# Kernel tuning notes

Hardware: AMD Instinct MI355X
Metric: run time of the kernel (lower is better)

Reference implementation:

```python
import jax, jax.numpy as jnp
import numpy as np

L, D, H, KV, HD, KVL, I, PL = 8, 2048, 8, 2, 256, 4096, 8192, 256
FULL = (4,)          # layers with full (global) attention / global RoPE
POS = 2047           # current decode position (cache write slot)
N_REP = H // KV      # GQA expansion factor


def rms(x, eps=1e-6):
    # RMSNorm without scale (v_norm); scale applied by caller where needed
    return x * jax.lax.rsqrt(jnp.mean(x * x, axis=-1, keepdims=True) + eps)


def rope(x, cos, sin):
    half = HD // 2
    rot = jnp.concatenate([-x[..., half:], x[..., :half]], axis=-1)
    return x * cos + rot * sin


def _rope_tables(theta):
    inv = 1.0 / (theta ** (np.arange(0, HD, 2, dtype=np.float32) / HD))
    ang = jnp.asarray(POS * inv, dtype=jnp.float32)
    return jnp.concatenate([jnp.cos(ang)] * 2), jnp.concatenate([jnp.sin(ang)] * 2)


def setup_inputs() -> dict:
    key = jax.random.key(0)
    ks = jax.random.split(key, 24)
    r = lambda k, s, sc=0.02: jax.random.normal(k, s, jnp.float32) * sc
    gains = lambda k, s: 1.0 + jax.random.normal(k, s, jnp.float32) * 0.02
    cos_s, sin_s = _rope_tables(10000.0)
    cos_f, sin_f = _rope_tables(1000000.0)
    um = jnp.zeros((1, 1, KVL, 1), jnp.float32).at[0, 0, POS, 0].set(1.0)
    mask = jnp.where(jnp.arange(KVL) <= POS, 0.0, -1e9).astype(jnp.float32)
    return {
        "hidden_states": r(ks[0], (1, 1, D), 1.0),
        "causal_mask": mask,
        "update_mask": um,
        "per_layer_combined": r(ks[1], (1, 1, L * PL), 1.0),
        "cos_s": cos_s, "sin_s": sin_s, "cos_f": cos_f, "sin_f": sin_f,
        "K_in": r(ks[2], (L, KV, KVL, HD)),
        "V_in": r(ks[3], (L, KV, KVL, HD)),
        "w_q": r(ks[4], (L, H * HD, D)),
        "w_k": r(ks[5], (L, KV * HD, D)),
        "w_v": r(ks[6], (L, KV * HD, D)),
        "w_o": r(ks[7], (L, D, H * HD)),
        "g_in_ln": gains(ks[8], (L, D)),
        "g_q_norm": gains(ks[9], (L, HD)),
        "g_k_norm": gains(ks[10], (L, HD)),
        "g_post_attn_ln": gains(ks[11], (L, D)),
        "g_pre_ff_ln": gains(ks[12], (L, D)),
        "g_post_ff_ln": gains(ks[13], (L, D)),
        "w_gate": r(ks[14], (L, I, D)),
        "w_up": r(ks[15], (L, I, D)),
        "w_down": r(ks[16], (L, D, I)),
        "w_plg": r(ks[17], (L, PL, D)),
        "w_plp": r(ks[18], (L, D, PL)),
        "g_post_pl_ln": gains(ks[19], (L, D)),
        "layer_scalar": jnp.ones((L,), jnp.float32),
    }


def reference(hidden_states, causal_mask, update_mask, per_layer_combined,
              cos_s, sin_s, cos_f, sin_f, K_in, V_in,
              w_q, w_k, w_v, w_o,
              g_in_ln, g_q_norm, g_k_norm, g_post_attn_ln, g_pre_ff_ln, g_post_ff_ln,
              w_gate, w_up, w_down, w_plg, w_plp, g_post_pl_ln, layer_scalar):
    um = update_mask[0, 0]          # [KVL,1] one-hot at write position
    h = hidden_states[0, 0]         # [D], batch=1/seq=1 decode
    K_outs, V_outs = [], []
    for i in range(L):
        cos, sin = (cos_f, sin_f) if i in FULL else (cos_s, sin_s)
        # --- attention block ---
        res = h
        x = rms(h) * g_in_ln[i]
        q = rms((w_q[i] @ x).reshape(H, HD)) * g_q_norm[i]
        q = rope(q, cos, sin)                                   # [H,HD]
        k = rms((w_k[i] @ x).reshape(KV, HD)) * g_k_norm[i]
        k = rope(k, cos, sin)                                   # [KV,HD]
        v = rms((w_v[i] @ x).reshape(KV, HD))                    # v_norm (no scale)
        # full-tensor masked blend = KV cache write (faithful to source)
        Ko = K_in[i] * (1.0 - um) + k[:, None, :] * um          # [KV,KVL,HD]
        Vo = V_in[i] * (1.0 - um) + v[:, None, :] * um
        K_outs.append(Ko); V_outs.append(Vo)
        Ke = jnp.repeat(Ko, N_REP, axis=0)                      # GQA expand [H,KVL,HD]
        Ve = jnp.repeat(Vo, N_REP, axis=0)
        scores = jnp.einsum('hd,hkd->hk', q, Ke) + causal_mask  # no 1/sqrt(hd) in source
        attn = jax.nn.softmax(scores, axis=-1)
        ao = jnp.einsum('hk,hkd->hd', attn, Ve).reshape(H * HD)
        ao = rms(w_o[i] @ ao) * g_post_attn_ln[i]
        h = res + ao
        # --- gated MLP ---
        res = h
        xm = rms(h) * g_pre_ff_ln[i]
        m = w_down[i] @ (jax.nn.gelu(w_gate[i] @ xm, approximate=True) * (w_up[i] @ xm))
        h = res + rms(m) * g_post_ff_ln[i]
        # --- per-layer input gating ---
        res = h
        pls = per_layer_combined[0, 0, i * PL:(i + 1) * PL]     # [PL]
        g = jax.nn.gelu(w_plg[i] @ h, approximate=True) * pls
        h = res + rms(w_plp[i] @ g) * g_post_pl_ln[i]
        h = h * layer_scalar[i]
    return (h[None, None, :], jnp.stack(K_outs), jnp.stack(V_outs))
```

## Files before the change

kernel.cpp:

```cpp
#include <hip/hip_runtime.h>

#define NL   8
#define DIM  2048
#define NH   8
#define NKV  2
#define HD   256
#define KVL  4096
#define FFI  8192
#define PLD  256
#define POS  2047
#define NCH  128
#define CP   16

__device__ __forceinline__ float dot4(float4 a, float4 b){
  return a.x*b.x + a.y*b.y + a.z*b.z + a.w*b.w;
}

__device__ __forceinline__ float waveAllSum(float v){
#pragma unroll
  for(int o=1;o<64;o<<=1) v += __shfl_xor(v,o,64);
  return v;
}

__device__ __forceinline__ float blockSum256(float v, float* red){
  int lane = threadIdx.x & 63, w = threadIdx.x >> 6;
  v = waveAllSum(v);
  __syncthreads();
  if(lane==0) red[w] = v;
  __syncthreads();
  return red[0]+red[1]+red[2]+red[3];
}

__device__ __forceinline__ float gelu_tanh(float v){
  return 0.5f*v*(1.0f + tanhf(0.7978845608028654f*(v + 0.044715f*v*v*v)));
}

__device__ __forceinline__ float4 normRope(const float* __restrict__ raw, int lane,
    const float* __restrict__ gain, const float* __restrict__ cosT,
    const float* __restrict__ sinT, bool doRope){
  float4 v4 = ((const float4*)raw)[lane];
  float ss = waveAllSum(dot4(v4,v4));
  float sc = rsqrtf(ss*(1.f/HD) + 1e-6f);
  float4 n;
  if(gain){
    float4 g4 = ((const float4*)gain)[lane];
    n.x=v4.x*sc*g4.x; n.y=v4.y*sc*g4.y; n.z=v4.z*sc*g4.z; n.w=v4.w*sc*g4.w;
  } else {
    n.x=v4.x*sc; n.y=v4.y*sc; n.z=v4.z*sc; n.w=v4.w*sc;
  }
  if(!doRope) return n;
  float4 np;
  np.x=__shfl_xor(n.x,32,64); np.y=__shfl_xor(n.y,32,64);
  np.z=__shfl_xor(n.z,32,64); np.w=__shfl_xor(n.w,32,64);
  float4 c4 = ((const float4*)cosT)[lane];
  float4 s4 = ((const float4*)sinT)[lane];
  float sg = (lane < 32) ? -1.f : 1.f;
  float4 o;
  o.x = n.x*c4.x + sg*np.x*s4.x;
  o.y = n.y*c4.y + sg*np.y*s4.y;
  o.z = n.z*c4.z + sg*np.z*s4.z;
  o.w = n.w*c4.w + sg*np.w*s4.w;
  return o;
}

__global__ __launch_bounds__(256) void qkv_k(
    const float* __restrict__ Wq, const float* __restrict__ Wk,
    const float* __restrict__ Wv,
    const float* __restrict__ hC, const float* __restrict__ u,
    const float* __restrict__ g_pl, const float* __restrict__ lsc,
    const float* __restrict__ g_in, const float* __restrict__ hidden,
    float* __restrict__ hA, float* __restrict__ qkv){
  __shared__ float xs[DIM];
  __shared__ float red[4];
  int tid = threadIdx.x;
  float hv[8];
  if(hidden){
#pragma unroll
    for(int i=0;i<8;i++) hv[i] = hidden[tid + i*256];
  } else {
    float uv[8]; float ss1 = 0.f;
#pragma unroll
    for(int i=0;i<8;i++){ uv[i] = u[tid + i*256]; ss1 += uv[i]*uv[i]; }
    ss1 = blockSum256(ss1, red);
    float r1 = rsqrtf(ss1*(1.f/DIM) + 1e-6f);
    float ls = lsc[0];
#pragma unroll
    for(int i=0;i<8;i++){
      int idx = tid + i*256;
      hv[i] = (hC[idx] + uv[i]*r1*g_pl[idx])*ls;
    }
  }
  float ss2 = 0.f;
#pragma unroll
  for(int i=0;i<8;i++) ss2 += hv[i]*hv[i];
  ss2 = blockSum256(ss2, red);
  float r2 = rsqrtf(ss2*(1.f/DIM) + 1e-6f);
#pragma unroll
  for(int i=0;i<8;i++){
    int idx = tid + i*256;
    xs[idx] = hv[i]*r2*g_in[idx];
    if(blockIdx.x==0) hA[idx] = hv[i];
  }
  __syncthreads();
  int lane = tid & 63, wv = tid >> 6;
  int r = blockIdx.x*4 + wv;
  const float* W; int row;
  if(r < 2048){ W = Wq; row = r; }
  else if(r < 2560){ W = Wk; row = r - 2048; }
  else { W = Wv; row = r - 2560; }
  const float4* Wr = (const float4*)(W + (size_t)row*DIM);
  const float4* xs4 = (const float4*)xs;
  float4 w8[8];
#pragma unroll
  for(int i=0;i<8;i++) w8[i] = Wr[i*64+lane];
  float acc = 0.f;
#pragma unroll
  for(int i=0;i<8;i++) acc += dot4(w8[i], xs4[i*64+lane]);
  acc = waveAllSum(acc);
  if(lane==0) qkv[r] = acc;
}

__global__ __launch_bounds__(256) void attn_k(
    const float* __restrict__ qkvb,
    const float* __restrict__ gq, const float* __restrict__ gk,
    const float* __restrict__ cosT, const float* __restrict__ sinT,
    float* __restrict__ Kl, float* __restrict__ Vl,
    float* __restrict__ pm, float* __restrict__ pl, float* __restrict__ po){
  int b = blockIdx.x, tid = threadIdx.x, lane = tid & 63, wv = tid >> 6;

  if(b == NKV*NCH){
    int kvv = wv >> 1, isV = wv & 1;
    const float* raw = qkvb + (isV ? 2560 : 2048) + kvv*HD;
    float4 o = normRope(raw, lane, isV ? nullptr : gk, cosT, sinT, !isV);
    float* dst = (isV ? Vl : Kl) + ((size_t)kvv*KVL + POS)*HD;
    ((float4*)dst)[lane] = o;
    return;
  }

  int kv = b & 1, c = b >> 1;
  __shared__ float q_s[4][HD];
  __shared__ float vf_s[HD];
  __shared__ float s_s[4][CP];
  __shared__ float s_w[4][CP];
  bool fresh = (c == NCH-1);

  {
    float4 o = normRope(qkvb + (kv*4 + wv)*HD, lane, gq, cosT, sinT, true);
    ((float4*)q_s[wv])[lane] = o;
  }
  float4 kf4 = {0,0,0,0};
  if(fresh){
    if(wv == 3) kf4 = normRope(qkvb + 2048 + kv*HD, lane, gk, cosT, sinT, true);
    if(wv == 1){
      float4 o = normRope(qkvb + 2560 + kv*HD, lane, nullptr, cosT, sinT, false);
      ((float4*)vf_s)[lane] = o;
    }
  }
  __syncthreads();

  float4 q4[4];
#pragma unroll
  for(int hh=0;hh<4;hh++) q4[hh] = ((const float4*)q_s[hh])[lane];
  const float4* Kp = (const float4*)(Kl + ((size_t)kv*KVL + c*CP)*HD);
#pragma unroll
  for(int j=0;j<4;j++){
    int p = wv*4 + j;
    float4 k4 = (fresh && p==CP-1) ? kf4 : Kp[(size_t)p*64 + lane];
    float d0 = dot4(k4,q4[0]), d1 = dot4(k4,q4[1]);
    float d2 = dot4(k4,q4[2]), d3 = dot4(k4,q4[3]);
    d0 = waveAllSum(d0); d1 = waveAllSum(d1);
    d2 = waveAllSum(d2); d3 = waveAllSum(d3);
    if(lane==0){ s_s[0][p]=d0; s_s[1][p]=d1; s_s[2][p]=d2; s_s[3][p]=d3; }
  }
  __syncthreads();

  if(tid < 64){
    int hh = tid >> 4, pp = tid & 15;
    float s = s_s[hh][pp];
    float m = s;
#pragma unroll
    for(int o=1;o<16;o<<=1) m = fmaxf(m, __shfl_xor(m,o,64));
    float e = __expf(s - m);
    float ls = e;
#pragma unroll
    for(int o=1;o<16;o<<=1) ls += __shfl_xor(ls,o,64);
    s_w[hh][pp] = e;
    if(pp==0){ int hg = kv*4 + hh; pm[hg*NCH + c] = m; pl[hg*NCH + c] = ls; }
  }
  __syncthreads();

  int d = tid;
  const float* Vp = Vl + ((size_t)kv*KVL + c*CP)*HD;
  float vv[CP];
#pragma unroll
  for(int p2=0;p2<CP;p2++) vv[p2] = Vp[(size_t)p2*HD + d];
  if(fresh) vv[CP-1] = vf_s[d];
  float acc[4] = {0.f,0.f,0.f,0.f};
#pragma unroll
  for(int p2=0;p2<CP;p2++){
#pragma unroll
    for(int hh=0;hh<4;hh++) acc[hh] += s_w[hh][p2]*vv[p2];
  }
#pragma unroll
  for(int hh=0;hh<4;hh++)
    po[((size_t)(kv*4+hh)*NCH + c)*HD + d] = acc[hh];
}

__global__ __launch_bounds__(256) void attn_c(const float* __restrict__ pm,
    const float* __restrict__ pl, const float* __restrict__ po, float* __restrict__ ao){
  int h = blockIdx.x, tid = threadIdx.x;
  __shared__ float sm[NCH], sl[NCH], se[NCH];
  if(tid < NCH){ sm[tid] = pm[h*NCH+tid]; sl[tid] = pl[h*NCH+tid]; }
  __syncthreads();
  float M = -1e30f;
  for(int c=0;c<NCH;c++) M = fmaxf(M, sm[c]);
  if(tid < NCH) se[tid] = __expf(sm[tid]-M);
  __syncthreads();
  float Lh = 0.f;
  for(int c=0;c<NCH;c++) Lh += sl[c]*se[c];
  float a0=0.f, a1=0.f, a2=0.f, a3=0.f;
#pragma unroll 1
  for(int c=0;c<NCH;c+=4){
    a0 += po[((size_t)h*NCH + c  )*HD + tid]*se[c];
    a1 += po[((size_t)h*NCH + c+1)*HD + tid]*se[c+1];
    a2 += po[((size_t)h*NCH + c+2)*HD + tid]*se[c+2];
    a3 += po[((size_t)h*NCH + c+3)*HD + tid]*se[c+3];
  }
  ao[h*HD + tid] = (a0+a1+a2+a3) / Lh;
}

template<int C>
__global__ __launch_bounds__(256) void gemv_k(const float* __restrict__ W,
    const float* __restrict__ x, float* __restrict__ y){
  __shared__ float xs[C];
  for(int i=threadIdx.x; i<C/4; i+=256)
    ((float4*)xs)[i] = ((const float4*)x)[i];
  __syncthreads();
  int lane = threadIdx.x & 63, wv = threadIdx.x >> 6;
  int r = blockIdx.x*4 + wv;
  const float4* Wr = (const float4*)(W + (size_t)r*C);
  const float4* xs4 = (const float4*)xs;
  float acc = 0.f;
#pragma unroll
  for(int ii=0;ii<C/2048;ii++){
    float4 w8[8];
#pragma unroll
    for(int i=0;i<8 && ii*8+i < C/256;i++) w8[i] = Wr[(ii*8+i)*64+lane];
#pragma unroll
    for(int i=0;i<8 && ii*8+i < C/256;i++) acc += dot4(w8[i], xs4[(ii*8+i)*64+lane]);
  }
  if(C < 2048){
    float4 w1 = Wr[lane];
    acc = dot4(w1, xs4[lane]);
  }
  acc = waveAllSum(acc);
  if(lane==0) y[r] = acc;
}

__global__ __launch_bounds__(256) void gateup_k(const float* __restrict__ Wg,
    const float* __restrict__ Wu, const float* __restrict__ y,
    const float* __restrict__ hA, const float* __restrict__ g_pa,
    const float* __restrict__ g_pf, float* __restrict__ hB, float* __restrict__ t){
  __shared__ float xs[DIM];
  __shared__ float red[4];
  int tid = threadIdx.x;
  float yv[8]; float ss1 = 0.f;
#pragma unroll
  for(int i=0;i<8;i++){ yv[i] = y[tid + i*256]; ss1 += yv[i]*yv[i]; }
  ss1 = blockSum256(ss1, red);
  float r1 = rsqrtf(ss1*(1.f/DIM) + 1e-6f);
  float hv[8]; float ss2 = 0.f;
#pragma unroll
  for(int i=0;i<8;i++){
    int idx = tid + i*256;
    hv[i] = hA[idx] + yv[i]*r1*g_pa[idx];
    ss2 += hv[i]*hv[i];
  }
  ss2 = blockSum256(ss2, red);
  float r2 = rsqrtf(ss2*(1.f/DIM) + 1e-6f);
#pragma unroll
  for(int i=0;i<8;i++){
    int idx = tid + i*256;
    xs[idx] = hv[i]*r2*g_pf[idx];
    if(blockIdx.x==0) hB[idx] = hv[i];
  }
  __syncthreads();
  int lane = tid & 63, wv = tid >> 6;
  int j = blockIdx.x*4 + wv;
  const float4* Gr = (const float4*)(Wg + (size_t)j*DIM);
  const float4* Ur = (const float4*)(Wu + (size_t)j*DIM);
  const float4* xs4 = (const float4*)xs;
  float4 g8[8], u8[8];
#pragma unroll
  for(int i=0;i<8;i++) g8[i] = Gr[i*64+lane];
#pragma unroll
  for(int i=0;i<8;i++) u8[i] = Ur[i*64+lane];
  float ag = 0.f, au = 0.f;
#pragma unroll
  for(int i=0;i<8;i++){
    float4 bv = xs4[i*64+lane];
    ag += dot4(g8[i], bv);
    au += dot4(u8[i], bv);
  }
  ag = waveAllSum(ag);
  au = waveAllSum(au);
  if(lane==0) t[j] = gelu_tanh(ag)*au;
}

__global__ __launch_bounds__(256) void down_k(const float* __restrict__ Wd,
    const float* __restrict__ t, float* __restrict__ mv){
  __shared__ float red[4];
  int tid = threadIdx.x, lane = tid & 63, wv = tid >> 6;
  int r = blockIdx.x;
  const float4* Wr = (const float4*)(Wd + (size_t)r*FFI) + wv*512;
  const float4* tp = (const float4*)t + wv*512;
  float4 w8[8], t8[8];
#pragma unroll
  for(int i=0;i<8;i++) w8[i] = Wr[i*64+lane];
#pragma unroll
  for(int i=0;i<8;i++) t8[i] = tp[i*64+lane];
  float acc = 0.f;
#pragma unroll
  for(int i=0;i<8;i++) acc += dot4(w8[i], t8[i]);
  acc = waveAllSum(acc);
  if(lane==0) red[wv] = acc;
  __syncthreads();
  if(tid==0) mv[r] = red[0]+red[1]+red[2]+red[3];
}

__global__ __launch_bounds__(256) void plg_k(const float* __restrict__ W,
    const float* __restrict__ mv, const float* __restrict__ hB,
    const float* __restrict__ g_ff, const float* __restrict__ pls,
    float* __restrict__ hCout, float* __restrict__ gb){
  __shared__ float xs[DIM];
  __shared__ float red[4];
  int tid = threadIdx.x;
  float mvv[8]; float ss1 = 0.f;
#pragma unroll
  for(int i=0;i<8;i++){ mvv[i] = mv[tid + i*256]; ss1 += mvv[i]*mvv[i]; }
  ss1 = blockSum256(ss1, red);
  float r1 = rsqrtf(ss1*(1.f/DIM) + 1e-6f);
#pragma unroll
  for(int i=0;i<8;i++){
    int idx = tid + i*256;
    float hc = hB[idx] + mvv[i]*r1*g_ff[idx];
    xs[idx] = hc;
    if(blockIdx.x==0) hCout[idx] = hc;
  }
  __syncthreads();
  int lane = tid & 63, wv = tid >> 6;
  int r = blockIdx.x*4 + wv;
  const float4* Wr = (const float4*)(W + (size_t)r*DIM);
  const float4* xs4 = (const float4*)xs;
  float4 w8[8];
#pragma unroll
  for(int i=0;i<8;i++) w8[i] = Wr[i*64+lane];
  float acc = 0.f;
#pragma unroll
  for(int i=0;i<8;i++) acc += dot4(w8[i], xs4[i*64+lane]);
  acc = waveAllSum(acc);
  if(lane==0) gb[r] = gelu_tanh(acc)*pls[r];
}

__global__ __launch_bounds__(256) void final_k(const float* __restrict__ u,
    const float* __restrict__ hC, const float* __restrict__ g_pl,
    const float* __restrict__ lsc, float* __restrict__ out){
  __shared__ float red[4];
  int tid = threadIdx.x;
  float uv[8]; float ss1 = 0.f;
#pragma unroll
  for(int i=0;i<8;i++){ uv[i] = u[tid + i*256]; ss1 += uv[i]*uv[i]; }
  ss1 = blockSum256(ss1, red);
  float r1 = rsqrtf(ss1*(1.f/DIM) + 1e-6f);
  float ls = lsc[0];
#pragma unroll
  for(int i=0;i<8;i++){
    int idx = tid + i*256;
    out[idx] = (hC[idx] + uv[i]*r1*g_pl[idx])*ls;
  }
}

extern "C" void kernel_launch(void* const* d_in, const int* in_sizes, int n_in,
                              void* d_out, int out_size, void* d_ws, size_t ws_size,
                              hipStream_t stream){
  const float* hidden   = (const float*)d_in[0];
  const float* plc      = (const float*)d_in[3];
  const float* cos_s    = (const float*)d_in[4];
  const float* sin_s    = (const float*)d_in[5];
  const float* cos_f    = (const float*)d_in[6];
  const float* sin_f    = (const float*)d_in[7];
  const float* K_in     = (const float*)d_in[8];
  const float* V_in     = (const float*)d_in[9];
  const float* w_q      = (const float*)d_in[10];
  const float* w_k      = (const float*)d_in[11];
  const float* w_v      = (const float*)d_in[12];
  const float* w_o      = (const float*)d_in[13];
  const float* g_in_ln  = (const float*)d_in[14];
  const float* g_q_norm = (const float*)d_in[15];
  const float* g_k_norm = (const float*)d_in[16];
  const float* g_pa_ln  = (const float*)d_in[17];
  const float* g_pf_ln  = (const float*)d_in[18];
  const float* g_ff_ln  = (const float*)d_in[19];
  const float* w_gate   = (const float*)d_in[20];
  const float* w_up     = (const float*)d_in[21];
  const float* w_down   = (const float*)d_in[22];
  const float* w_plg    = (const float*)d_in[23];
  const float* w_plp    = (const float*)d_in[24];
  const float* g_pl_ln  = (const float*)d_in[25];
  const float* l_scal   = (const float*)d_in[26];

  float* out  = (float*)d_out;
  float* outK = out + DIM;
  float* outV = outK + (size_t)NL*NKV*KVL*HD;

  float* ws   = (float*)d_ws;
  float* hA   = ws;
  float* hB   = ws + 2048;
  float* hC   = ws + 4096;
  float* qkvb = ws + 6144;
  float* y    = ws + 9216;
  float* t    = ws + 11264;
  float* mv   = ws + 19456;
  float* gb   = ws + 21504;
  float* u    = ws + 21760;
  float* pm   = ws + 23808;
  float* pl   = ws + 24832;
  float* po   = ws + 25856;
  float* ao   = ws + 288000;

  (void)hipMemcpyAsync(outK, K_in, (size_t)NL*NKV*KVL*HD*sizeof(float),
                       hipMemcpyDeviceToDevice, stream);
  (void)hipMemcpyAsync(outV, V_in, (size_t)NL*NKV*KVL*HD*sizeof(float),
                       hipMemcpyDeviceToDevice, stream);

  for(int l=0;l<NL;l++){
    const float* cosT = (l==4) ? cos_f : cos_s;
    const float* sinT = (l==4) ? sin_f : sin_s;
    float* Kl = outK + (size_t)l*NKV*KVL*HD;
    float* Vl = outV + (size_t)l*NKV*KVL*HD;

    qkv_k<<<768,256,0,stream>>>(
        w_q + (size_t)l*NH*HD*DIM, w_k + (size_t)l*NKV*HD*DIM,
        w_v + (size_t)l*NKV*HD*DIM,
        hC, u,
        (l>0) ? g_pl_ln + (size_t)(l-1)*DIM : g_pl_ln,
        (l>0) ? l_scal + (l-1) : l_scal,
        g_in_ln + (size_t)l*DIM,
        (l==0) ? hidden : nullptr,
        hA, qkvb);

    attn_k<<<NKV*NCH+1,256,0,stream>>>(qkvb, g_q_norm + l*HD, g_k_norm + l*HD,
                                       cosT, sinT, Kl, Vl, pm, pl, po);

    attn_c<<<NH,256,0,stream>>>(pm, pl, po, ao);

    gemv_k<DIM><<<512,256,0,stream>>>(w_o + (size_t)l*DIM*NH*HD, ao, y);

    gateup_k<<<FFI/4,256,0,stream>>>(w_gate + (size_t)l*FFI*DIM,
                                     w_up + (size_t)l*FFI*DIM,
                                     y, hA, g_pa_ln + (size_t)l*DIM,
                                     g_pf_ln + (size_t)l*DIM, hB, t);

    down_k<<<DIM,256,0,stream>>>(w_down + (size_t)l*DIM*FFI, t, mv);

    plg_k<<<PLD/4,256,0,stream>>>(w_plg + (size_t)l*PLD*DIM, mv, hB,
                                  g_ff_ln + (size_t)l*DIM, plc + l*PLD, hC, gb);

    gemv_k<PLD><<<512,256,0,stream>>>(w_plp + (size_t)l*DIM*PLD, gb, u);
  }

  final_k<<<1,256,0,stream>>>(u, hC, g_pl_ln + (size_t)(NL-1)*DIM,
                              l_scal + (NL-1), out);
}
```

Before: 809.2 us.

## Fuse KV-cache copy into attention kernel instead of upfront device memcpy

Drops the two full-cache device-to-device memcpys. The attention blocks now read K/V rows straight from the input cache and write them to the output cache as they go. Extra blocks appended to the attention grid copy the unused second half of each layer's cache using nontemporal loads and stores. This avoids reading the first half of the cache twice, but it adds copy work and per-layer store traffic inside the attention kernel, which sits on the critical path. Residual buffers are also renamed for clarity.

Result: faster. 787.8 us, median of 2 (-2.6%).

```diff
diff --git a/kernel.cpp b/kernel.cpp
--- a/kernel.cpp
+++ b/kernel.cpp
@@ -12,8 +12,19 @@
 #define NCH  128
 #define CP   16
 
+typedef float vfloat4 __attribute__((ext_vector_type(4)));
+
 __device__ __forceinline__ float dot4(float4 a, float4 b){
   return a.x*b.x + a.y*b.y + a.z*b.z + a.w*b.w;
+}
+
+__device__ __forceinline__ float4 ntld4(const float4* p){
+  vfloat4 v = __builtin_nontemporal_load((const vfloat4*)p);
+  float4 r; r.x=v.x; r.y=v.y; r.z=v.z; r.w=v.w; return r;
+}
+__device__ __forceinline__ void ntst4(float4* p, float4 v){
+  vfloat4 t; t.x=v.x; t.y=v.y; t.z=v.z; t.w=v.w;
+  __builtin_nontemporal_store(t, (vfloat4*)p);
 }
 
 __device__ __forceinline__ float waveAllSum(float v){
@@ -66,10 +77,10 @@
 __global__ __launch_bounds__(256) void qkv_k(
     const float* __restrict__ Wq, const float* __restrict__ Wk,
     const float* __restrict__ Wv,
-    const float* __restrict__ hC, const float* __restrict__ u,
+    const float* __restrict__ hFF, const float* __restrict__ u,
     const float* __restrict__ g_pl, const float* __restrict__ lsc,
     const float* __restrict__ g_in, const float* __restrict__ hidden,
-    float* __restrict__ hA, float* __restrict__ qkv){
+    float* __restrict__ hRes, float* __restrict__ qkv){
   __shared__ float xs[DIM];
   __shared__ float red[4];
   int tid = threadIdx.x;
@@ -87,7 +98,7 @@
 #pragma unroll
     for(int i=0;i<8;i++){
       int idx = tid + i*256;
-      hv[i] = (hC[idx] + uv[i]*r1*g_pl[idx])*ls;
+      hv[i] = (hFF[idx] + uv[i]*r1*g_pl[idx])*ls;
     }
   }
   float ss2 = 0.f;
@@ -99,7 +110,7 @@
   for(int i=0;i<8;i++){
     int idx = tid + i*256;
     xs[idx] = hv[i]*r2*g_in[idx];
-    if(blockIdx.x==0) hA[idx] = hv[i];
+    if(blockIdx.x==0) hRes[idx] = hv[i];
   }
   __syncthreads();
   int lane = tid & 63, wv = tid >> 6;
@@ -124,6 +135,7 @@
     const float* __restrict__ qkvb,
     const float* __restrict__ gq, const float* __restrict__ gk,
     const float* __restrict__ cosT, const float* __restrict__ sinT,
+    const float* __restrict__ Ki, const float* __restrict__ Vi,
     float* __restrict__ Kl, float* __restrict__ Vl,
     float* __restrict__ pm, float* __restrict__ pl, float* __restrict__ po){
   int b = blockIdx.x, tid = threadIdx.x, lane = tid & 63, wv = tid >> 6;
@@ -136,6 +148,20 @@
     ((float4*)dst)[lane] = o;
     return;
   }
+  if(b > NKV*NCH){
+    int b2 = b - (NKV*NCH+1);
+#pragma unroll
+    for(int i=0;i<8;i++){
+      int ri = b2*32 + wv*8 + i;
+      int combo = ri >> 11;
+      int pos = 2048 + (ri & 2047);
+      size_t off = ((size_t)(combo&1)*KVL + pos)*HD;
+      const float4* s = (const float4*)(((combo>>1) ? Vi : Ki) + off);
+      float4* d = (float4*)(((combo>>1) ? Vl : Kl) + off);
+      ntst4(d + lane, ntld4(s + lane));
+    }
+    return;
+  }
 
   int kv = b & 1, c = b >> 1;
   __shared__ float q_s[4][HD];
@@ -144,10 +170,8 @@
   __shared__ float s_w[4][CP];
   bool fresh = (c == NCH-1);
 
-  {
-    float4 o = normRope(qkvb + (kv*4 + wv)*HD, lane, gq, cosT, sinT, true);
-    ((float4*)q_s[wv])[lane] = o;
-  }
+  { float4 o = normRope(qkvb + (kv*4 + wv)*HD, lane, gq, cosT, sinT, true);
+    ((float4*)q_s[wv])[lane] = o; }
   float4 kf4 = {0,0,0,0};
   if(fresh){
     if(wv == 3) kf4 = normRope(qkvb + 2048 + kv*HD, lane, gk, cosT, sinT, true);
@@ -161,11 +185,18 @@
   float4 q4[4];
 #pragma unroll
   for(int hh=0;hh<4;hh++) q4[hh] = ((const float4*)q_s[hh])[lane];
-  const float4* Kp = (const float4*)(Kl + ((size_t)kv*KVL + c*CP)*HD);
+  const float4* Kp = (const float4*)(Ki + ((size_t)kv*KVL + c*CP)*HD);
+  float4* Kd = (float4*)(Kl + ((size_t)kv*KVL + c*CP)*HD);
 #pragma unroll
   for(int j=0;j<4;j++){
     int p = wv*4 + j;
-    float4 k4 = (fresh && p==CP-1) ? kf4 : Kp[(size_t)p*64 + lane];
+    bool isFreshRow = (fresh && p==CP-1);
+    float4 k4;
+    if(isFreshRow) k4 = kf4;
+    else {
+      k4 = Kp[(size_t)p*64 + lane];
+      ntst4(Kd + (size_t)p*64 + lane, k4);
+    }
     float d0 = dot4(k4,q4[0]), d1 = dot4(k4,q4[1]);
     float d2 = dot4(k4,q4[2]), d3 = dot4(k4,q4[3]);
     d0 = waveAllSum(d0); d1 = waveAllSum(d1);
@@ -190,11 +221,18 @@
   __syncthreads();
 
   int d = tid;
-  const float* Vp = Vl + ((size_t)kv*KVL + c*CP)*HD;
+  const float* Vp = Vi + ((size_t)kv*KVL + c*CP)*HD;
+  float* Vd = Vl + ((size_t)kv*KVL + c*CP)*HD;
   float vv[CP];
 #pragma unroll
-  for(int p2=0;p2<CP;p2++) vv[p2] = Vp[(size_t)p2*HD + d];
-  if(fresh) vv[CP-1] = vf_s[d];
+  for(int p2=0;p2<CP;p2++){
+    bool isFreshRow = (fresh && p2==CP-1);
+    if(isFreshRow) vv[p2] = vf_s[d];
+    else {
+      vv[p2] = Vp[(size_t)p2*HD + d];
+      Vd[(size_t)p2*HD + d] = vv[p2];
+    }
+  }
   float acc[4] = {0.f,0.f,0.f,0.f};
 #pragma unroll
   for(int p2=0;p2<CP;p2++){
@@ -259,8 +297,8 @@
 
 __global__ __launch_bounds__(256) void gateup_k(const float* __restrict__ Wg,
     const float* __restrict__ Wu, const float* __restrict__ y,
-    const float* __restrict__ hA, const float* __restrict__ g_pa,
-    const float* __restrict__ g_pf, float* __restrict__ hB, float* __restrict__ t){
+    const float* __restrict__ hRes, const float* __restrict__ g_pa,
+    const float* __restrict__ g_pf, float* __restrict__ hMid, float* __restrict__ t){
   __shared__ float xs[DIM];
   __shared__ float red[4];
   int tid = threadIdx.x;
@@ -273,7 +311,7 @@
 #pragma unroll
   for(int i=0;i<8;i++){
     int idx = tid + i*256;
-    hv[i] = hA[idx] + yv[i]*r1*g_pa[idx];
+    hv[i] = hRes[idx] + yv[i]*r1*g_pa[idx];
     ss2 += hv[i]*hv[i];
   }
   ss2 = blockSum256(ss2, red);
@@ -282,7 +320,7 @@
   for(int i=0;i<8;i++){
     int idx = tid + i*256;
     xs[idx] = hv[i]*r2*g_pf[idx];
-    if(blockIdx.x==0) hB[idx] = hv[i];
+    if(blockIdx.x==0) hMid[idx] = hv[i];
   }
   __syncthreads();
   int lane = tid & 63, wv = tid >> 6;
@@ -329,9 +367,9 @@
 }
 
 __global__ __launch_bounds__(256) void plg_k(const float* __restrict__ W,
-    const float* __restrict__ mv, const float* __restrict__ hB,
+    const float* __restrict__ mv, const float* __restrict__ hMid,
     const float* __restrict__ g_ff, const float* __restrict__ pls,
-    float* __restrict__ hCout, float* __restrict__ gb){
+    float* __restrict__ hFFout, float* __restrict__ gb){
   __shared__ float xs[DIM];
   __shared__ float red[4];
   int tid = threadIdx.x;
@@ -343,9 +381,9 @@
 #pragma unroll
   for(int i=0;i<8;i++){
     int idx = tid + i*256;
-    float hc = hB[idx] + mvv[i]*r1*g_ff[idx];
+    float hc = hMid[idx] + mvv[i]*r1*g_ff[idx];
     xs[idx] = hc;
-    if(blockIdx.x==0) hCout[idx] = hc;
+    if(blockIdx.x==0) hFFout[idx] = hc;
   }
   __syncthreads();
   int lane = tid & 63, wv = tid >> 6;
@@ -363,7 +401,7 @@
 }
 
 __global__ __launch_bounds__(256) void final_k(const float* __restrict__ u,
-    const float* __restrict__ hC, const float* __restrict__ g_pl,
+    const float* __restrict__ hFF, const float* __restrict__ g_pl,
     const float* __restrict__ lsc, float* __restrict__ out){
   __shared__ float red[4];
   int tid = threadIdx.x;
@@ -376,7 +414,7 @@
 #pragma unroll
   for(int i=0;i<8;i++){
     int idx = tid + i*256;
-    out[idx] = (hC[idx] + uv[i]*r1*g_pl[idx])*ls;
+    out[idx] = (hFF[idx] + uv[i]*r1*g_pl[idx])*ls;
   }
 }
 
@@ -414,9 +452,9 @@
   float* outV = outK + (size_t)NL*NKV*KVL*HD;
 
   float* ws   = (float*)d_ws;
-  float* hA   = ws;
-  float* hB   = ws + 2048;
-  float* hC   = ws + 4096;
+  float* hRes = ws;
+  float* hMid = ws + 2048;
+  float* hFF  = ws + 4096;
   float* qkvb = ws + 6144;
   float* y    = ws + 9216;
   float* t    = ws + 11264;
@@ -428,29 +466,27 @@
   float* po   = ws + 25856;
   float* ao   = ws + 288000;
 
-  (void)hipMemcpyAsync(outK, K_in, (size_t)NL*NKV*KVL*HD*sizeof(float),
-                       hipMemcpyDeviceToDevice, stream);
-  (void)hipMemcpyAsync(outV, V_in, (size_t)NL*NKV*KVL*HD*sizeof(float),
-                       hipMemcpyDeviceToDevice, stream);
-
   for(int l=0;l<NL;l++){
     const float* cosT = (l==4) ? cos_f : cos_s;
     const float* sinT = (l==4) ? sin_f : sin_s;
     float* Kl = outK + (size_t)l*NKV*KVL*HD;
     float* Vl = outV + (size_t)l*NKV*KVL*HD;
+    const float* Ki = K_in + (size_t)l*NKV*KVL*HD;
+    const float* Vi = V_in + (size_t)l*NKV*KVL*HD;
 
     qkv_k<<<768,256,0,stream>>>(
         w_q + (size_t)l*NH*HD*DIM, w_k + (size_t)l*NKV*HD*DIM,
         w_v + (size_t)l*NKV*HD*DIM,
-        hC, u,
+        hFF, u,
         (l>0) ? g_pl_ln + (size_t)(l-1)*DIM : g_pl_ln,
         (l>0) ? l_scal + (l-1) : l_scal,
         g_in_ln + (size_t)l*DIM,
         (l==0) ? hidden : nullptr,
-        hA, qkvb);
-
-    attn_k<<<NKV*NCH+1,256,0,stream>>>(qkvb, g_q_norm + l*HD, g_k_norm + l*HD,
-                                       cosT, sinT, Kl, Vl, pm, pl, po);
+        hRes, qkvb);
+
+    attn_k<<<NKV*NCH+1+256,256,0,stream>>>(qkvb, g_q_norm + l*HD,
+                                           g_k_norm + l*HD, cosT, sinT,
+                                           Ki, Vi, Kl, Vl, pm, pl, po);
 
     attn_c<<<NH,256,0,stream>>>(pm, pl, po, ao);
 
@@ -458,17 +494,17 @@
 
     gateup_k<<<FFI/4,256,0,stream>>>(w_gate + (size_t)l*FFI*DIM,
                                      w_up + (size_t)l*FFI*DIM,
-                                     y, hA, g_pa_ln + (size_t)l*DIM,
-                                     g_pf_ln + (size_t)l*DIM, hB, t);
+                                     y, hRes, g_pa_ln + (size_t)l*DIM,
+                                     g_pf_ln + (size_t)l*DIM, hMid, t);
 
     down_k<<<DIM,256,0,stream>>>(w_down + (size_t)l*DIM*FFI, t, mv);
 
-    plg_k<<<PLD/4,256,0,stream>>>(w_plg + (size_t)l*PLD*DIM, mv, hB,
-                                  g_ff_ln + (size_t)l*DIM, plc + l*PLD, hC, gb);
+    plg_k<<<PLD/4,256,0,stream>>>(w_plg + (size_t)l*PLD*DIM, mv, hMid,
+                                  g_ff_ln + (size_t)l*DIM, plc + l*PLD, hFF, gb);
 
     gemv_k<PLD><<<512,256,0,stream>>>(w_plp + (size_t)l*DIM*PLD, gb, u);
   }
 
-  final_k<<<1,256,0,stream>>>(u, hC, g_pl_ln + (size_t)(NL-1)*DIM,
+  final_k<<<1,256,0,stream>>>(u, hFF, g_pl_ln + (size_t)(NL-1)*DIM,
                               l_scal + (NL-1), out);
 }
```
